# Kernel optimization log

Hardware: AMD Instinct MI355X
Metric: run time of the kernel (lower is better)

The kernel has to match this reference:

```python
import jax, jax.numpy as jnp
import numpy as np
import math

B, S, D, H, TD = 256, 200, 64, 512, 8


def setup_inputs():
    key = jax.random.key(0)
    ks = jax.random.split(key, 12)
    sd, sh, so = 1.0 / math.sqrt(D), 1.0 / math.sqrt(H), 1.0 / math.sqrt(H + TD)
    return dict(
        x=jax.random.normal(ks[0], (B, S, D), jnp.float32),
        a=jax.random.normal(ks[3], (B, TD), jnp.float32),
        t=jnp.cumsum(jax.random.uniform(ks[2], (B, S), jnp.float32), axis=1),
        mask=(jax.random.uniform(ks[1], (B, S, D)) < 0.8).astype(jnp.float32),
        w_dg_x=jax.random.normal(ks[4], (D,), jnp.float32) * sd,
        b_dg_x=jnp.zeros((D,), jnp.float32),
        W_dg_h=jax.random.normal(ks[5], (H, D), jnp.float32) * sd,
        b_dg_h=jnp.zeros((H,), jnp.float32),
        W=jax.random.normal(ks[6], (3 * H, D), jnp.float32) * sd,
        U=jax.random.normal(ks[7], (3 * H, H), jnp.float32) * sh,
        V=jax.random.normal(ks[8], (3 * H, D), jnp.float32) * sd,
        b=jnp.zeros((3 * H,), jnp.float32),
        attn_v=jnp.ones((H,), jnp.float32),
        W_out=jax.random.normal(ks[9], (H, H + TD), jnp.float32) * so,
        b_out=jnp.zeros((H,), jnp.float32),
    )


def reference(x, a, t, mask, w_dg_x, b_dg_x, W_dg_h, b_dg_h, W, U, V, b, attn_v, W_out, b_out):
    # ---- GRU-D preprocessing: per-feature time gaps delta ----
    x_tm = jnp.transpose(x, (1, 0, 2))    # (S,B,D) time-major
    m_tm = jnp.transpose(mask, (1, 0, 2))
    dt = jnp.diff(t, axis=1, prepend=t[:, :1])      # (B,S), dt[0]=0
    dt_tm = jnp.transpose(dt)[:, :, None]           # (S,B,1)
    # delta[i] = dt[i] + (1 - mask[i-1]) * delta[i-1]; ones at step 0 -> delta[0]=0
    m_prev = jnp.concatenate([jnp.ones((1,) + m_tm.shape[1:], m_tm.dtype), m_tm[:-1]], axis=0)

    def delta_step(d, inp):
        dt_i, mp_i = inp
        d = dt_i + (1.0 - mp_i) * d
        return d, d

    _, delta_tm = jax.lax.scan(delta_step, jnp.zeros((B, D), x.dtype), (dt_tm, m_prev))

    # empirical mean of observed values for imputation
    x_mean = (mask * x).sum((0, 1)) / jnp.maximum(mask.sum((0, 1)), 1.0)  # (D,)

    Wz, Wr, Wh = W[:H], W[H:2 * H], W[2 * H:]
    Uz, Ur, Uh = U[:H], U[H:2 * H], U[2 * H:]
    Vz, Vr, Vh = V[:H], V[H:2 * H], V[2 * H:]
    bz, br, bh = b[:H], b[H:2 * H], b[2 * H:]

    def cell(carry, inp):
        h, x_last = carry
        x_i, m_i, d_i = inp                                        # (B,D) each
        gamma_x = jnp.exp(-jax.nn.relu(w_dg_x * d_i + b_dg_x))     # (B,D) input decay
        gamma_h = jnp.exp(-jax.nn.relu(d_i @ W_dg_h.T + b_dg_h))   # (B,H) hidden decay
        x_hat = m_i * x_i + (1.0 - m_i) * (gamma_x * x_last + (1.0 - gamma_x) * x_mean)
        h_dec = gamma_h * h
        z = jax.nn.sigmoid(x_hat @ Wz.T + h_dec @ Uz.T + m_i @ Vz.T + bz)
        r = jax.nn.sigmoid(x_hat @ Wr.T + h_dec @ Ur.T + m_i @ Vr.T + br)
        h_til = jnp.tanh(x_hat @ Wh.T + (r * h_dec) @ Uh.T + m_i @ Vh.T + bh)
        h_new = (1.0 - z) * h_dec + z * h_til
        x_last_new = m_i * x_i + (1.0 - m_i) * x_last
        return (h_new, x_last_new), h_new

    init = (jnp.zeros((B, H), x.dtype), jnp.zeros((B, D), x.dtype))
    _, h_all = jax.lax.scan(cell, init, (x_tm, m_tm, delta_tm))    # (S,B,H)

    # ---- attention pooling over time (softmax along seq dim, as in torch dim=0) ----
    score = (h_all @ attn_v) / math.sqrt(H)        # (S,B)
    w_attn = jax.nn.softmax(score, axis=0)
    attn_h = (h_all * w_attn[..., None]).sum(0)    # (B,H)

    # ---- treatment head ----
    return jnp.concatenate([attn_h, a], axis=1) @ W_out.T + b_out  # (B,H)
```

## Files before the change

### kernel.cpp

```cpp
#include <hip/hip_runtime.h>
#include <hip/hip_bf16.h>
#include <stdint.h>


typedef unsigned short u16;
typedef unsigned int   u32;
typedef unsigned long long u64;
typedef short bfrag  __attribute__((ext_vector_type(8)));
typedef u16   u16x8  __attribute__((ext_vector_type(8)));
typedef float f32x4  __attribute__((ext_vector_type(4)));

#define NB 256
#define NS 200
#define ND 64
#define NH 512

#define MFMA(a,b,c) __builtin_amdgcn_mfma_f32_16x16x32_bf16((a),(b),(c),0,0,0)

union UQ { u16x8 h; bfrag s; u64 u[2]; uint4 q; };

__device__ __forceinline__ float b2f(u16 v){ union { float f; u32 u; } c; c.u = ((u32)v) << 16; return c.f; }
__device__ __forceinline__ u16 f2b(float f){ union { float f; u32 u; } c; c.f = f; u32 r = c.u + 0x7FFFu + ((c.u >> 16) & 1u); return (u16)(r >> 16); }
__device__ __forceinline__ float sigm(float x){ return 1.f / (1.f + __expf(-x)); }
__device__ __forceinline__ float tanh_f(float x){ return 1.f - 2.f / (1.f + __expf(2.f * x)); }

__device__ __forceinline__ u64 cload64(const void* p){
  return __hip_atomic_load((const u64*)p, __ATOMIC_RELAXED, __HIP_MEMORY_SCOPE_AGENT);
}
__device__ __forceinline__ void cstore64(void* p, u64 v){
  __hip_atomic_store((u64*)p, v, __ATOMIC_RELAXED, __HIP_MEMORY_SCOPE_AGENT);
}
__device__ __forceinline__ u32 cload32(const u32* p){
  return __hip_atomic_load(p, __ATOMIC_RELAXED, __HIP_MEMORY_SCOPE_AGENT);
}
__device__ __forceinline__ void cstore32(u32* p, u32 v){
  __hip_atomic_store(p, v, __ATOMIC_RELAXED, __HIP_MEMORY_SCOPE_AGENT);
}
__device__ __forceinline__ bool poll_ge(const u32* wp, u32 tgt){
  int fuel = 1 << 19;
  while (true) {
    u32 v = cload32(wp);
    if (__all(v >= tgt)) return true;
    __builtin_amdgcn_s_sleep(1);
    if (--fuel == 0) return false;
  }
}
__device__ __forceinline__ bfrag ldfrag(const float* src){
  f32x4 lo = *(const f32x4*)src;
  f32x4 hi = *(const f32x4*)(src + 4);
  UQ z;
  z.h[0]=f2b(lo[0]); z.h[1]=f2b(lo[1]); z.h[2]=f2b(lo[2]); z.h[3]=f2b(lo[3]);
  z.h[4]=f2b(hi[0]); z.h[5]=f2b(hi[1]); z.h[6]=f2b(hi[2]); z.h[7]=f2b(hi[3]);
  return z.s;
}
__device__ __forceinline__ void stage_bf16(u16* dst, const u16* src, int tid, bool zero){
  const int row = tid >> 4, sc = (tid & 15) * 32;
  u16* dp = &dst[((sc >> 3) * 16 + row) * 8];
  if (!zero) {
    const u16* hs = src + (size_t)row * 512 + sc;
    u64 a0 = cload64(hs),      a1 = cload64(hs + 4),  a2 = cload64(hs + 8),  a3 = cload64(hs + 12);
    u64 a4 = cload64(hs + 16), a5 = cload64(hs + 20), a6 = cload64(hs + 24), a7 = cload64(hs + 28);
    *(u64*)(dp)       = a0; *(u64*)(dp + 4)   = a1;
    *(u64*)(dp + 128) = a2; *(u64*)(dp + 132) = a3;
    *(u64*)(dp + 256) = a4; *(u64*)(dp + 260) = a5;
    *(u64*)(dp + 384) = a6; *(u64*)(dp + 388) = a7;
  } else {
    *(u64*)(dp)       = 0; *(u64*)(dp + 4)   = 0;
    *(u64*)(dp + 128) = 0; *(u64*)(dp + 132) = 0;
    *(u64*)(dp + 256) = 0; *(u64*)(dp + 260) = 0;
    *(u64*)(dp + 384) = 0; *(u64*)(dp + 388) = 0;
  }
}


__global__ void transpose_k(const float* __restrict__ Wout, float* __restrict__ WT){
  int i = blockIdx.x * 256 + threadIdx.x;
  if (i < 520 * 512) { int k = i >> 9, ho = i & 511; WT[i] = Wout[ho * 520 + k]; }
}

__global__ void mean1_k(const float* __restrict__ x, const float* __restrict__ mask,
                        float* __restrict__ PX, float* __restrict__ PM){
  int s = blockIdx.x, tid = threadIdx.x;
  __shared__ float lx[256], lm[256];
  float xa = 0.f, ma = 0.f;
  for (int i = tid; i < NB * ND; i += 256) {
    int b = i >> 6, d = i & 63;
    size_t ix = ((size_t)b * NS + s) * 64 + d;
    float m = mask[ix];
    xa += m * x[ix]; ma += m;
  }
  lx[tid] = xa; lm[tid] = ma;
  __syncthreads();
  if (tid < 64) {
    PX[(size_t)s * 64 + tid] = lx[tid] + lx[tid + 64] + lx[tid + 128] + lx[tid + 192];
    PM[(size_t)s * 64 + tid] = lm[tid] + lm[tid + 64] + lm[tid + 128] + lm[tid + 192];
  }
}

__global__ void mean2_k(const float* __restrict__ PX, const float* __restrict__ PM,
                        float* __restrict__ XMEAN){
  int d = threadIdx.x;
  float sx = 0.f, sm = 0.f;
  for (int s = 0; s < NS; ++s){ sx += PX[s * 64 + d]; sm += PM[s * 64 + d]; }
  XMEAN[d] = sx / fmaxf(sm, 1.f);
}

__global__ void prep_k(const float* __restrict__ x, const float* __restrict__ mask,
                       const float* __restrict__ tc, const float* __restrict__ wdgx,
                       const float* __restrict__ bdgx, const float* __restrict__ XMEAN,
                       u16* __restrict__ XHAT, u16* __restrict__ MASKB, u16* __restrict__ DELTA){
  int g = blockIdx.x * 256 + threadIdx.x;
  int b = g >> 6, d = g & 63;
  float xmean = XMEAN[d], wx = wdgx[d], bx = bdgx[d];
  float xl = 0.f, del = 0.f, tprev = 0.f, mprev = 1.f;
  for (int s = 0; s < NS; ++s){
    float tv = tc[b * NS + s];
    float dtv = (s == 0) ? 0.f : (tv - tprev);
    tprev = tv;
    del = dtv + (1.f - mprev) * del;
    size_t ix = ((size_t)b * NS + s) * 64 + d;
    float m = mask[ix], xv = x[ix];
    float gx = __expf(-fmaxf(0.f, wx * del + bx));
    float xh = m * xv + (1.f - m) * (gx * xl + (1.f - gx) * xmean);
    size_t ox = ((size_t)s * NB + b) * 64 + d;
    XHAT[ox] = f2b(xh); MASKB[ox] = f2b(m); DELTA[ox] = f2b(del);
    xl = m * xv + (1.f - m) * xl;
    mprev = m;
  }
}

__global__ void xpart_k(const float* __restrict__ Wm, const float* __restrict__ Vm,
                        const float* __restrict__ bv, const u16* __restrict__ XHAT,
                        const u16* __restrict__ MASKB, u16* __restrict__ XP){
  const int tid = threadIdx.x, lane = tid & 63, wid = tid >> 6;
  const int l16 = lane & 15, krow = lane >> 4, r4 = lane >> 2, cb = (lane & 3) * 8;
  const int chunk = blockIdx.x >> 1, p = blockIdx.x & 1;
  const int R0 = chunk * 128;
  const int wbase = p * 768 + wid * 192;
  __shared__ u16 panel[16 * 16 * 8];
  __shared__ float xb[4][16 * 35];
  float* xw = xb[wid];
  const f32x4 Z4 = {0.f, 0.f, 0.f, 0.f};

  bfrag BW[12][2], BV2[12][2];
  #pragma unroll
  for (int ct = 0; ct < 12; ++ct)
    #pragma unroll
    for (int kx = 0; kx < 2; ++kx) {
      BW[ct][kx]  = ldfrag(Wm + (size_t)(wbase + ct * 16 + l16) * 64 + kx * 32 + krow * 8);
      BV2[ct][kx] = ldfrag(Vm + (size_t)(wbase + ct * 16 + l16) * 64 + kx * 32 + krow * 8);
    }
  float bias6[6][8];
  #pragma unroll
  for (int grp = 0; grp < 6; ++grp)
    #pragma unroll
    for (int q = 0; q < 8; ++q) bias6[grp][q] = bv[wbase + grp * 32 + cb + q];

  for (int it = 0; it < 8; ++it) {
    const int R = R0 + it * 16;
    { const int kb = tid >> 4, row = tid & 15;
      const u16* sp = (kb < 8 ? XHAT : MASKB) + (size_t)(R + row) * 64 + (kb & 7) * 8;
      *(uint4*)&panel[(kb * 16 + row) * 8] = *(const uint4*)sp; }
    __syncthreads();
    u16* orow_ = XP + (size_t)(R + r4) * 1536 + wbase;
    #pragma unroll
    for (int grp = 0; grp < 6; ++grp) {
      f32x4 ac0 = Z4, ac1 = Z4;
      #pragma unroll
      for (int kx = 0; kx < 2; ++kx) {
        bfrag ax = *(const bfrag*)&panel[((kx * 4 + krow) * 16 + l16) * 8];
        ac0 = MFMA(ax, BW[grp*2][kx], ac0); ac1 = MFMA(ax, BW[grp*2+1][kx], ac1);
        bfrag am = *(const bfrag*)&panel[((8 + kx * 4 + krow) * 16 + l16) * 8];
        ac0 = MFMA(am, BV2[grp*2][kx], ac0); ac1 = MFMA(am, BV2[grp*2+1][kx], ac1);
      }
      #pragma unroll
      for (int j = 0; j < 4; ++j) { xw[(krow*4+j)*35 + l16] = ac0[j]; xw[(krow*4+j)*35 + 16 + l16] = ac1[j]; }
      UQ ov;
      #pragma unroll
      for (int q = 0; q < 8; ++q) ov.h[q] = f2b(xw[r4 * 35 + cb + q] + bias6[grp][q]);
      *(u64*)(orow_ + grp * 32 + cb) = ov.u[0];
      *(u64*)(orow_ + grp * 32 + cb + 4) = ov.u[1];
    }
    __syncthreads();
  }
}

__global__ __launch_bounds__(256, 1) void grud_rnn(
    const float* __restrict__ Um, const float* __restrict__ Wdg, const float* __restrict__ bdg,
    const u16* __restrict__ XP, const u16* __restrict__ DELTA,
    u16* __restrict__ HDECB, u16* __restrict__ RHB, u16* __restrict__ HALL,
    u32* __restrict__ flags)
{
  const int tid = threadIdx.x, lane = tid & 63, wid = tid >> 6, bid = blockIdx.x;
  const int lid = (bid & 7) * 8 + (bid >> 3);
  const int rb = lid >> 2, g = lid & 3, m0 = rb * 16;
  const int l16 = lane & 15, krow = lane >> 4, r4 = lane >> 2, cb = (lane & 3) * 8;
  const int pw = g * 4 + wid;
  const int cw = g * 128 + wid * 32;
  u32* FB = flags + rb * 32;

  __shared__ u16 hpan[64 * 16 * 8];
  __shared__ u16 rpan[64 * 16 * 8];
  __shared__ u16 dpan[8 * 16 * 8];
  __shared__ float xb[4][16 * 34];
  __shared__ int s_ab;
  float* xw = xb[wid];
  const f32x4 Z4 = {0.f, 0.f, 0.f, 0.f};
  if (tid == 0) s_ab = 0;
  __syncthreads();

  bfrag BZ[16][2], BR[16][2], BH[16][2], BG[2][2];
  #pragma unroll
  for (int kk = 0; kk < 16; ++kk) {
    const size_t ko = (size_t)(kk * 32 + krow * 8);
    #pragma unroll
    for (int t2 = 0; t2 < 2; ++t2) {
      BZ[kk][t2] = ldfrag(Um + (size_t)(       cw + t2 * 16 + l16) * 512 + ko);
      BR[kk][t2] = ldfrag(Um + (size_t)(512  + cw + t2 * 16 + l16) * 512 + ko);
      BH[kk][t2] = ldfrag(Um + (size_t)(1024 + cw + t2 * 16 + l16) * 512 + ko);
    }
  }
  #pragma unroll
  for (int kk = 0; kk < 2; ++kk)
    #pragma unroll
    for (int t2 = 0; t2 < 2; ++t2)
      BG[kk][t2] = ldfrag(Wdg + (size_t)(cw + t2 * 16 + l16) * 64 + kk * 32 + krow * 8);
  float gb8[8];
  #pragma unroll
  for (int q = 0; q < 8; ++q) gb8[q] = bdg[cw + cb + q];

  const int slot = ((cw + cb) >> 3) * 16 + r4;

  for (int t = 0; t < NS; ++t) {
    const int tn = (t + 1 < NS) ? t + 1 : NS - 1;
    const u16* xp = XP + ((size_t)t * NB + m0 + r4) * 1536 + cw + cb;
    u64 xz0 = *(const u64*)(xp),        xz1 = *(const u64*)(xp + 4);
    u64 xr0 = *(const u64*)(xp + 512),  xr1 = *(const u64*)(xp + 516);
    u64 xh0 = *(const u64*)(xp + 1024), xh1 = *(const u64*)(xp + 1028);
    if (tid < 128) {
      const int kb = tid >> 4, row = tid & 15;
      const u16* sp = DELTA + ((size_t)tn * NB + m0 + row) * 64 + kb * 8;
      *(uint4*)&dpan[(kb * 16 + row) * 8] = *(const uint4*)sp;
    }
    if (wid == 0 && t > 0) { if (!poll_ge(FB + (lane & 15), (u32)t)) s_ab = 1; }
    __syncthreads();
    if (s_ab) break;
    stage_bf16(hpan, HDECB + (size_t)m0 * 512, tid, t == 0);
    __syncthreads();
    f32x4 aR0 = Z4, aR1 = Z4;
    #pragma unroll
    for (int kk = 0; kk < 16; ++kk) {
      bfrag a = *(const bfrag*)&hpan[((kk * 4 + krow) * 16 + l16) * 8];
      aR0 = MFMA(a, BR[kk][0], aR0); aR1 = MFMA(a, BR[kk][1], aR1);
    }
    #pragma unroll
    for (int j = 0; j < 4; ++j) { xw[(krow*4+j)*34 + l16] = aR0[j]; xw[(krow*4+j)*34 + 16 + l16] = aR1[j]; }
    UQ hd_; hd_.h = *(const u16x8*)&hpan[slot * 8];
    UQ xr_; xr_.u[0] = xr0; xr_.u[1] = xr1;
    UQ rh_;
    #pragma unroll
    for (int q = 0; q < 8; ++q) {
      float rv = sigm(b2f(xr_.h[q]) + xw[r4 * 34 + cb + q]);
      rh_.h[q] = f2b(rv * b2f(hd_.h[q]));
    }
    u16* rdst = RHB + (size_t)(m0 + r4) * 512 + cw + cb;
    cstore64(rdst, rh_.u[0]); cstore64(rdst + 4, rh_.u[1]);
    asm volatile("s_waitcnt vmcnt(0)" ::: "memory");
    if (lane == 0) cstore32(FB + 16 + pw, (u32)(t + 1));
    f32x4 aZ0 = Z4, aZ1 = Z4;
    #pragma unroll
    for (int kk = 0; kk < 16; ++kk) {
      bfrag a = *(const bfrag*)&hpan[((kk * 4 + krow) * 16 + l16) * 8];
      aZ0 = MFMA(a, BZ[kk][0], aZ0); aZ1 = MFMA(a, BZ[kk][1], aZ1);
    }
    #pragma unroll
    for (int j = 0; j < 4; ++j) { xw[(krow*4+j)*34 + l16] = aZ0[j]; xw[(krow*4+j)*34 + 16 + l16] = aZ1[j]; }
    UQ xz_; xz_.u[0] = xz0; xz_.u[1] = xz1;
    float zf[8];
    #pragma unroll
    for (int q = 0; q < 8; ++q) zf[q] = sigm(b2f(xz_.h[q]) + xw[r4 * 34 + cb + q]);
    f32x4 g0 = Z4, g1 = Z4;
    #pragma unroll
    for (int kk = 0; kk < 2; ++kk) {
      bfrag a = *(const bfrag*)&dpan[((kk * 4 + krow) * 16 + l16) * 8];
      g0 = MFMA(a, BG[kk][0], g0); g1 = MFMA(a, BG[kk][1], g1);
    }
    #pragma unroll
    for (int j = 0; j < 4; ++j) { xw[(krow*4+j)*34 + l16] = g0[j]; xw[(krow*4+j)*34 + 16 + l16] = g1[j]; }
    float gm8[8];
    #pragma unroll
    for (int q = 0; q < 8; ++q)
      gm8[q] = __expf(-fmaxf(0.f, xw[r4 * 34 + cb + q] + gb8[q]));
    if (wid == 0) { if (!poll_ge(FB + 16 + (lane & 15), (u32)(t + 1))) s_ab = 1; }
    __syncthreads();
    if (s_ab) break;
    stage_bf16(rpan, RHB + (size_t)m0 * 512, tid, false);
    __syncthreads();
    f32x4 aH0 = Z4, aH1 = Z4;
    #pragma unroll
    for (int kk = 0; kk < 16; ++kk) {
      bfrag a = *(const bfrag*)&rpan[((kk * 4 + krow) * 16 + l16) * 8];
      aH0 = MFMA(a, BH[kk][0], aH0); aH1 = MFMA(a, BH[kk][1], aH1);
    }
    #pragma unroll
    for (int j = 0; j < 4; ++j) { xw[(krow*4+j)*34 + l16] = aH0[j]; xw[(krow*4+j)*34 + 16 + l16] = aH1[j]; }
    UQ xh_; xh_.u[0] = xh0; xh_.u[1] = xh1;
    UQ hw_, hdn_;
    #pragma unroll
    for (int q = 0; q < 8; ++q) {
      float til = tanh_f(b2f(xh_.h[q]) + xw[r4 * 34 + cb + q]);
      float hn = (1.f - zf[q]) * b2f(hd_.h[q]) + zf[q] * til;
      hw_.h[q] = f2b(hn);
      hdn_.h[q] = f2b(gm8[q] * hn);
    }
    if (t + 1 < NS) {
      u16* hdst = HDECB + (size_t)(m0 + r4) * 512 + cw + cb;
      cstore64(hdst, hdn_.u[0]); cstore64(hdst + 4, hdn_.u[1]);
    }
    asm volatile("s_waitcnt vmcnt(0)" ::: "memory");
    if (lane == 0) cstore32(FB + 0 + pw, (u32)(t + 1));
    u16* hp = HALL + ((size_t)t * NB + m0 + r4) * 512 + cw + cb;
    *(u64*)hp = hw_.u[0]; *(u64*)(hp + 4) = hw_.u[1];
    __syncthreads();
  }
}


__global__ void attn_k(const u16* __restrict__ HALL, const float* __restrict__ av,
                       float* __restrict__ ATTN){
  const int b = blockIdx.x, tid = threadIdx.x, lane = tid & 63, wid = tid >> 6;
  __shared__ float avs[512], wgt[256], red[8];
  for (int i = tid; i < 512; i += 256) avs[i] = av[i];
  __syncthreads();
  float val = -3.0e38f;
  if (tid < NS) {
    const u16* hp = HALL + ((size_t)tid * NB + b) * 512;
    float acc = 0.f;
    for (int h = 0; h < 512; h += 8) {
      UQ w; w.q = *(const uint4*)(hp + h);
      #pragma unroll
      for (int j = 0; j < 8; ++j) acc += b2f(w.h[j]) * avs[h + j];
    }
    val = acc * 0.04419417382415922f;
  }
  float m = val;
  #pragma unroll
  for (int off = 32; off; off >>= 1) m = fmaxf(m, __shfl_xor(m, off, 64));
  if (lane == 0) red[wid] = m;
  __syncthreads();
  m = fmaxf(fmaxf(red[0], red[1]), fmaxf(red[2], red[3]));
  float e = (tid < NS) ? __expf(val - m) : 0.f;
  float sum = e;
  #pragma unroll
  for (int off = 32; off; off >>= 1) sum += __shfl_xor(sum, off, 64);
  if (lane == 0) red[4 + wid] = sum;
  __syncthreads();
  const float ssum = red[4] + red[5] + red[6] + red[7];
  wgt[tid] = e / ssum;
  __syncthreads();
  float a0 = 0.f, a1 = 0.f;
  const int h0 = tid * 2;
  for (int s = 0; s < NS; ++s) {
    float w = wgt[s];
    u32 pr = *(const u32*)(HALL + ((size_t)s * NB + b) * 512 + h0);
    a0 += w * b2f((u16)(pr & 0xFFFFu));
    a1 += w * b2f((u16)(pr >> 16));
  }
  ATTN[(size_t)b * 512 + h0] = a0;
  ATTN[(size_t)b * 512 + h0 + 1] = a1;
}

__global__ void out_k(const float* __restrict__ ATTN, const float* __restrict__ Ain,
                      const float* __restrict__ WT, const float* __restrict__ bout,
                      float* __restrict__ OUT){
  const int g = blockIdx.x, tid = threadIdx.x;
  __shared__ float ah[4][520];
  for (int i = tid; i < 4 * 520; i += 256) {
    int bb = i / 520, k = i % 520;
    int b = g * 4 + bb;
    ah[bb][k] = (k < 512) ? ATTN[(size_t)b * 512 + k] : Ain[b * 8 + (k - 512)];
  }
  __syncthreads();
  #pragma unroll
  for (int part = 0; part < 2; ++part) {
    const int ho = part * 256 + tid;
    float a0 = bout[ho], a1 = a0, a2 = a0, a3 = a0;
    for (int k = 0; k < 520; ++k) {
      float w = WT[(size_t)k * 512 + ho];
      a0 += ah[0][k] * w; a1 += ah[1][k] * w; a2 += ah[2][k] * w; a3 += ah[3][k] * w;
    }
    OUT[(size_t)(g * 4 + 0) * 512 + ho] = a0;
    OUT[(size_t)(g * 4 + 1) * 512 + ho] = a1;
    OUT[(size_t)(g * 4 + 2) * 512 + ho] = a2;
    OUT[(size_t)(g * 4 + 3) * 512 + ho] = a3;
  }
}


extern "C" void kernel_launch(void* const* d_in, const int* in_sizes, int n_in,
                              void* d_out, int out_size, void* d_ws, size_t ws_size,
                              hipStream_t stream) {
  (void)in_sizes; (void)n_in; (void)out_size; (void)ws_size;
  const float* x    = (const float*)d_in[0];
  const float* a_in = (const float*)d_in[1];
  const float* tc   = (const float*)d_in[2];
  const float* mask = (const float*)d_in[3];
  const float* wdgx = (const float*)d_in[4];
  const float* bdgx = (const float*)d_in[5];
  const float* Wdgh = (const float*)d_in[6];
  const float* bdgh = (const float*)d_in[7];
  const float* Wm   = (const float*)d_in[8];
  const float* Um   = (const float*)d_in[9];
  const float* Vm   = (const float*)d_in[10];
  const float* bvv  = (const float*)d_in[11];
  const float* attv = (const float*)d_in[12];
  const float* Wout = (const float*)d_in[13];
  const float* bout = (const float*)d_in[14];

  char* ws = (char*)d_ws;
  size_t o = 0;
  auto al = [&](size_t sz) { size_t r = o; o += (sz + 255) & ~(size_t)255; return r; };
  u32*   flags = (u32*)  (ws + al(16 * 32 * 4));
  float* XMEAN = (float*)(ws + al(256));
  float* PX    = (float*)(ws + al((size_t)NS * 64 * 4));
  float* PM    = (float*)(ws + al((size_t)NS * 64 * 4));
  u16*   XHAT  = (u16*)  (ws + al((size_t)NS * NB * 64 * 2));
  u16*   MASKB = (u16*)  (ws + al((size_t)NS * NB * 64 * 2));
  u16*   DELTA = (u16*)  (ws + al((size_t)NS * NB * 64 * 2));
  u16*   HDECB = (u16*)  (ws + al((size_t)NB * NH * 2));
  u16*   RHB   = (u16*)  (ws + al((size_t)NB * NH * 2));
  u16*   XP    = (u16*)  (ws + al((size_t)NS * NB * 1536 * 2));
  u16*   HALL  = (u16*)  (ws + al((size_t)NS * NB * NH * 2));
  float* ATTN  = (float*)(ws + al((size_t)NB * NH * 4));
  float* WT    = (float*)(ws + al((size_t)520 * 512 * 4));

  hipMemsetAsync(flags, 0, 16 * 32 * 4, stream);

  transpose_k<<<(520 * 512 + 255) / 256, 256, 0, stream>>>(Wout, WT);
  mean1_k<<<NS, 256, 0, stream>>>(x, mask, PX, PM);
  mean2_k<<<1, 64, 0, stream>>>(PX, PM, XMEAN);
  prep_k<<<NB * ND / 256, 256, 0, stream>>>(x, mask, tc, wdgx, bdgx, XMEAN, XHAT, MASKB, DELTA);
  xpart_k<<<800, 256, 0, stream>>>(Wm, Vm, bvv, XHAT, MASKB, XP);
  grud_rnn<<<64, 256, 0, stream>>>(Um, Wdgh, bdgh, XP, DELTA, HDECB, RHB, HALL, flags);
  attn_k<<<NB, 256, 0, stream>>>(HALL, attv, ATTN);
  out_k<<<64, 256, 0, stream>>>(ATTN, a_in, WT, bout, (float*)d_out);
}
```

Measured before the change: 2.174 ms.

## Split z-gate GEMM onto dedicated blocks and read h/r panels directly from global

The persistent GRU-D recurrence kernel grows from 64 to 96 blocks. Per 16-row batch group, four blocks handle the r and candidate gates, and two new blocks compute the z gate in parallel, publishing it through a global buffer guarded by flags. Hidden and reset panels are stored pre-swizzled in MFMA fragment order and loaded straight into registers, which removes LDS staging and its barriers. Flag polling also drops the sleep instruction. The r/h blocks now wait on the z blocks before the candidate step, and the extra flag traffic could lengthen the critical path.

```diff
diff --git a/kernel.cpp b/kernel.cpp
--- a/kernel.cpp
+++ b/kernel.cpp
@@ -37,11 +37,10 @@
   __hip_atomic_store(p, v, __ATOMIC_RELAXED, __HIP_MEMORY_SCOPE_AGENT);
 }
 __device__ __forceinline__ bool poll_ge(const u32* wp, u32 tgt){
-  int fuel = 1 << 19;
+  int fuel = 1 << 18;
   while (true) {
     u32 v = cload32(wp);
     if (__all(v >= tgt)) return true;
-    __builtin_amdgcn_s_sleep(1);
     if (--fuel == 0) return false;
   }
 }
@@ -52,24 +51,6 @@
   z.h[0]=f2b(lo[0]); z.h[1]=f2b(lo[1]); z.h[2]=f2b(lo[2]); z.h[3]=f2b(lo[3]);
   z.h[4]=f2b(hi[0]); z.h[5]=f2b(hi[1]); z.h[6]=f2b(hi[2]); z.h[7]=f2b(hi[3]);
   return z.s;
-}
-__device__ __forceinline__ void stage_bf16(u16* dst, const u16* src, int tid, bool zero){
-  const int row = tid >> 4, sc = (tid & 15) * 32;
-  u16* dp = &dst[((sc >> 3) * 16 + row) * 8];
-  if (!zero) {
-    const u16* hs = src + (size_t)row * 512 + sc;
-    u64 a0 = cload64(hs),      a1 = cload64(hs + 4),  a2 = cload64(hs + 8),  a3 = cload64(hs + 12);
-    u64 a4 = cload64(hs + 16), a5 = cload64(hs + 20), a6 = cload64(hs + 24), a7 = cload64(hs + 28);
-    *(u64*)(dp)       = a0; *(u64*)(dp + 4)   = a1;
-    *(u64*)(dp + 128) = a2; *(u64*)(dp + 132) = a3;
-    *(u64*)(dp + 256) = a4; *(u64*)(dp + 260) = a5;
-    *(u64*)(dp + 384) = a6; *(u64*)(dp + 388) = a7;
-  } else {
-    *(u64*)(dp)       = 0; *(u64*)(dp + 4)   = 0;
-    *(u64*)(dp + 128) = 0; *(u64*)(dp + 132) = 0;
-    *(u64*)(dp + 256) = 0; *(u64*)(dp + 260) = 0;
-    *(u64*)(dp + 384) = 0; *(u64*)(dp + 388) = 0;
-  }
 }
 
 
@@ -188,140 +169,199 @@
 __global__ __launch_bounds__(256, 1) void grud_rnn(
     const float* __restrict__ Um, const float* __restrict__ Wdg, const float* __restrict__ bdg,
     const u16* __restrict__ XP, const u16* __restrict__ DELTA,
-    u16* __restrict__ HDECB, u16* __restrict__ RHB, u16* __restrict__ HALL,
-    u32* __restrict__ flags)
+    u16* __restrict__ HP, u16* __restrict__ RP, u16* __restrict__ ZZB,
+    u16* __restrict__ HALL, u32* __restrict__ flags)
 {
   const int tid = threadIdx.x, lane = tid & 63, wid = tid >> 6, bid = blockIdx.x;
-  const int lid = (bid & 7) * 8 + (bid >> 3);
-  const int rb = lid >> 2, g = lid & 3, m0 = rb * 16;
+  const int lid = (bid & 7) * 12 + (bid >> 3);
+  const int rb = lid / 6, role = lid % 6, m0 = rb * 16;
   const int l16 = lane & 15, krow = lane >> 4, r4 = lane >> 2, cb = (lane & 3) * 8;
-  const int pw = g * 4 + wid;
-  const int cw = g * 128 + wid * 32;
-  u32* FB = flags + rb * 32;
-
-  __shared__ u16 hpan[64 * 16 * 8];
-  __shared__ u16 rpan[64 * 16 * 8];
-  __shared__ u16 dpan[8 * 16 * 8];
-  __shared__ float xb[4][16 * 34];
-  __shared__ int s_ab;
+  u32* FB = flags + rb * 64;
+  u16* HPr = HP + rb * 8192;
+  u16* RPr = RP + rb * 8192;
+
+  __shared__ float xb[4][16 * 68];
   float* xw = xb[wid];
   const f32x4 Z4 = {0.f, 0.f, 0.f, 0.f};
-  if (tid == 0) s_ab = 0;
-  __syncthreads();
-
-  bfrag BZ[16][2], BR[16][2], BH[16][2], BG[2][2];
-  #pragma unroll
-  for (int kk = 0; kk < 16; ++kk) {
-    const size_t ko = (size_t)(kk * 32 + krow * 8);
-    #pragma unroll
-    for (int t2 = 0; t2 < 2; ++t2) {
-      BZ[kk][t2] = ldfrag(Um + (size_t)(       cw + t2 * 16 + l16) * 512 + ko);
-      BR[kk][t2] = ldfrag(Um + (size_t)(512  + cw + t2 * 16 + l16) * 512 + ko);
-      BH[kk][t2] = ldfrag(Um + (size_t)(1024 + cw + t2 * 16 + l16) * 512 + ko);
-    }
-  }
-  #pragma unroll
-  for (int kk = 0; kk < 2; ++kk)
-    #pragma unroll
-    for (int t2 = 0; t2 < 2; ++t2)
-      BG[kk][t2] = ldfrag(Wdg + (size_t)(cw + t2 * 16 + l16) * 64 + kk * 32 + krow * 8);
-  float gb8[8];
-  #pragma unroll
-  for (int q = 0; q < 8; ++q) gb8[q] = bdg[cw + cb + q];
-
-  const int slot = ((cw + cb) >> 3) * 16 + r4;
-
-  for (int t = 0; t < NS; ++t) {
-    const int tn = (t + 1 < NS) ? t + 1 : NS - 1;
-    const u16* xp = XP + ((size_t)t * NB + m0 + r4) * 1536 + cw + cb;
-    u64 xz0 = *(const u64*)(xp),        xz1 = *(const u64*)(xp + 4);
-    u64 xr0 = *(const u64*)(xp + 512),  xr1 = *(const u64*)(xp + 516);
-    u64 xh0 = *(const u64*)(xp + 1024), xh1 = *(const u64*)(xp + 1028);
-    if (tid < 128) {
-      const int kb = tid >> 4, row = tid & 15;
-      const u16* sp = DELTA + ((size_t)tn * NB + m0 + row) * 64 + kb * 8;
-      *(uint4*)&dpan[(kb * 16 + row) * 8] = *(const uint4*)sp;
-    }
-    if (wid == 0 && t > 0) { if (!poll_ge(FB + (lane & 15), (u32)t)) s_ab = 1; }
-    __syncthreads();
-    if (s_ab) break;
-    stage_bf16(hpan, HDECB + (size_t)m0 * 512, tid, t == 0);
-    __syncthreads();
-    f32x4 aR0 = Z4, aR1 = Z4;
+
+  if (role < 4) {
+    const int pw = role * 4 + wid;
+    const int cw = role * 128 + wid * 32;
+    const int slotp = ((cw + cb) >> 3) * 16 + r4;
+    bfrag BR[16][2], BH[16][2], BG[2][2];
     #pragma unroll
     for (int kk = 0; kk < 16; ++kk) {
-      bfrag a = *(const bfrag*)&hpan[((kk * 4 + krow) * 16 + l16) * 8];
-      aR0 = MFMA(a, BR[kk][0], aR0); aR1 = MFMA(a, BR[kk][1], aR1);
-    }
-    #pragma unroll
-    for (int j = 0; j < 4; ++j) { xw[(krow*4+j)*34 + l16] = aR0[j]; xw[(krow*4+j)*34 + 16 + l16] = aR1[j]; }
-    UQ hd_; hd_.h = *(const u16x8*)&hpan[slot * 8];
-    UQ xr_; xr_.u[0] = xr0; xr_.u[1] = xr1;
-    UQ rh_;
-    #pragma unroll
-    for (int q = 0; q < 8; ++q) {
-      float rv = sigm(b2f(xr_.h[q]) + xw[r4 * 34 + cb + q]);
-      rh_.h[q] = f2b(rv * b2f(hd_.h[q]));
-    }
-    u16* rdst = RHB + (size_t)(m0 + r4) * 512 + cw + cb;
-    cstore64(rdst, rh_.u[0]); cstore64(rdst + 4, rh_.u[1]);
-    asm volatile("s_waitcnt vmcnt(0)" ::: "memory");
-    if (lane == 0) cstore32(FB + 16 + pw, (u32)(t + 1));
-    f32x4 aZ0 = Z4, aZ1 = Z4;
-    #pragma unroll
-    for (int kk = 0; kk < 16; ++kk) {
-      bfrag a = *(const bfrag*)&hpan[((kk * 4 + krow) * 16 + l16) * 8];
-      aZ0 = MFMA(a, BZ[kk][0], aZ0); aZ1 = MFMA(a, BZ[kk][1], aZ1);
-    }
-    #pragma unroll
-    for (int j = 0; j < 4; ++j) { xw[(krow*4+j)*34 + l16] = aZ0[j]; xw[(krow*4+j)*34 + 16 + l16] = aZ1[j]; }
-    UQ xz_; xz_.u[0] = xz0; xz_.u[1] = xz1;
-    float zf[8];
-    #pragma unroll
-    for (int q = 0; q < 8; ++q) zf[q] = sigm(b2f(xz_.h[q]) + xw[r4 * 34 + cb + q]);
-    f32x4 g0 = Z4, g1 = Z4;
-    #pragma unroll
-    for (int kk = 0; kk < 2; ++kk) {
-      bfrag a = *(const bfrag*)&dpan[((kk * 4 + krow) * 16 + l16) * 8];
-      g0 = MFMA(a, BG[kk][0], g0); g1 = MFMA(a, BG[kk][1], g1);
-    }
-    #pragma unroll
-    for (int j = 0; j < 4; ++j) { xw[(krow*4+j)*34 + l16] = g0[j]; xw[(krow*4+j)*34 + 16 + l16] = g1[j]; }
-    float gm8[8];
-    #pragma unroll
-    for (int q = 0; q < 8; ++q)
-      gm8[q] = __expf(-fmaxf(0.f, xw[r4 * 34 + cb + q] + gb8[q]));
-    if (wid == 0) { if (!poll_ge(FB + 16 + (lane & 15), (u32)(t + 1))) s_ab = 1; }
-    __syncthreads();
-    if (s_ab) break;
-    stage_bf16(rpan, RHB + (size_t)m0 * 512, tid, false);
-    __syncthreads();
-    f32x4 aH0 = Z4, aH1 = Z4;
-    #pragma unroll
-    for (int kk = 0; kk < 16; ++kk) {
-      bfrag a = *(const bfrag*)&rpan[((kk * 4 + krow) * 16 + l16) * 8];
-      aH0 = MFMA(a, BH[kk][0], aH0); aH1 = MFMA(a, BH[kk][1], aH1);
-    }
-    #pragma unroll
-    for (int j = 0; j < 4; ++j) { xw[(krow*4+j)*34 + l16] = aH0[j]; xw[(krow*4+j)*34 + 16 + l16] = aH1[j]; }
-    UQ xh_; xh_.u[0] = xh0; xh_.u[1] = xh1;
-    UQ hw_, hdn_;
-    #pragma unroll
-    for (int q = 0; q < 8; ++q) {
-      float til = tanh_f(b2f(xh_.h[q]) + xw[r4 * 34 + cb + q]);
-      float hn = (1.f - zf[q]) * b2f(hd_.h[q]) + zf[q] * til;
-      hw_.h[q] = f2b(hn);
-      hdn_.h[q] = f2b(gm8[q] * hn);
-    }
-    if (t + 1 < NS) {
-      u16* hdst = HDECB + (size_t)(m0 + r4) * 512 + cw + cb;
-      cstore64(hdst, hdn_.u[0]); cstore64(hdst + 4, hdn_.u[1]);
-    }
-    asm volatile("s_waitcnt vmcnt(0)" ::: "memory");
-    if (lane == 0) cstore32(FB + 0 + pw, (u32)(t + 1));
-    u16* hp = HALL + ((size_t)t * NB + m0 + r4) * 512 + cw + cb;
-    *(u64*)hp = hw_.u[0]; *(u64*)(hp + 4) = hw_.u[1];
-    __syncthreads();
+      const size_t ko = (size_t)(kk * 32 + krow * 8);
+      #pragma unroll
+      for (int t2 = 0; t2 < 2; ++t2) {
+        BR[kk][t2] = ldfrag(Um + (size_t)(512  + cw + t2 * 16 + l16) * 512 + ko);
+        BH[kk][t2] = ldfrag(Um + (size_t)(1024 + cw + t2 * 16 + l16) * 512 + ko);
+      }
+    }
+    #pragma unroll
+    for (int kk = 0; kk < 2; ++kk)
+      #pragma unroll
+      for (int t2 = 0; t2 < 2; ++t2)
+        BG[kk][t2] = ldfrag(Wdg + (size_t)(cw + t2 * 16 + l16) * 64 + kk * 32 + krow * 8);
+    float gb8[8];
+    #pragma unroll
+    for (int q = 0; q < 8; ++q) gb8[q] = bdg[cw + cb + q];
+
+    UQ hd_; hd_.u[0] = 0; hd_.u[1] = 0;
+
+    for (int t = 0; t < NS; ++t) {
+      const int tn = (t + 1 < NS) ? t + 1 : NS - 1;
+      const u16* xp = XP + ((size_t)t * NB + m0 + r4) * 1536 + cw + cb;
+      u64 xr0 = *(const u64*)(xp + 512),  xr1 = *(const u64*)(xp + 516);
+      u64 xh0 = *(const u64*)(xp + 1024), xh1 = *(const u64*)(xp + 1028);
+      const u16* dpp = DELTA + ((size_t)tn * NB + m0 + l16) * 64 + krow * 8;
+      UQ DA[2];
+      DA[0].u[0] = *(const u64*)(dpp);      DA[0].u[1] = *(const u64*)(dpp + 4);
+      DA[1].u[0] = *(const u64*)(dpp + 32); DA[1].u[1] = *(const u64*)(dpp + 36);
+      if (t > 0) { if (!poll_ge(FB + (lane & 15), (u32)t)) return; }
+      UQ A[16];
+      if (t > 0) {
+        #pragma unroll
+        for (int kk = 0; kk < 16; ++kk) {
+          const u16* p = HPr + (size_t)(kk * 64 + krow * 16 + l16) * 8;
+          A[kk].u[0] = cload64(p); A[kk].u[1] = cload64(p + 4);
+        }
+      } else {
+        #pragma unroll
+        for (int kk = 0; kk < 16; ++kk) { A[kk].u[0] = 0; A[kk].u[1] = 0; }
+      }
+      f32x4 aR0 = Z4, aR1 = Z4;
+      #pragma unroll
+      for (int kk = 0; kk < 16; ++kk) {
+        aR0 = MFMA(A[kk].s, BR[kk][0], aR0); aR1 = MFMA(A[kk].s, BR[kk][1], aR1);
+      }
+      #pragma unroll
+      for (int j = 0; j < 4; ++j) { xw[(krow*4+j)*68 + l16] = aR0[j]; xw[(krow*4+j)*68 + 16 + l16] = aR1[j]; }
+      UQ xr_; xr_.u[0] = xr0; xr_.u[1] = xr1;
+      UQ rh_;
+      #pragma unroll
+      for (int q = 0; q < 8; ++q) {
+        float rv = sigm(b2f(xr_.h[q]) + xw[r4 * 68 + cb + q]);
+        rh_.h[q] = f2b(rv * b2f(hd_.h[q]));
+      }
+      { u16* rdst = RPr + (size_t)slotp * 8;
+        cstore64(rdst, rh_.u[0]); cstore64(rdst + 4, rh_.u[1]); }
+      asm volatile("s_waitcnt vmcnt(0)" ::: "memory");
+      if (lane == 0) cstore32(FB + 16 + pw, (u32)(t + 1));
+      f32x4 g0 = Z4, g1 = Z4;
+      #pragma unroll
+      for (int kk = 0; kk < 2; ++kk) {
+        g0 = MFMA(DA[kk].s, BG[kk][0], g0); g1 = MFMA(DA[kk].s, BG[kk][1], g1);
+      }
+      #pragma unroll
+      for (int j = 0; j < 4; ++j) { xw[(krow*4+j)*68 + l16] = g0[j]; xw[(krow*4+j)*68 + 16 + l16] = g1[j]; }
+      float gm8[8];
+      #pragma unroll
+      for (int q = 0; q < 8; ++q)
+        gm8[q] = __expf(-fmaxf(0.f, xw[r4 * 68 + cb + q] + gb8[q]));
+      { const u32* wp; u32 tg = (u32)(t + 1);
+        if (lane < 16)      wp = FB + 16 + lane;
+        else if (lane < 24) wp = FB + 32 + (lane - 16);
+        else                wp = FB + 16;
+        if (!poll_ge(wp, tg)) return; }
+      u64 zz0 = cload64(ZZB + (size_t)(m0 + r4) * 512 + cw + cb);
+      u64 zz1 = cload64(ZZB + (size_t)(m0 + r4) * 512 + cw + cb + 4);
+      #pragma unroll
+      for (int kk = 0; kk < 16; ++kk) {
+        const u16* p = RPr + (size_t)(kk * 64 + krow * 16 + l16) * 8;
+        A[kk].u[0] = cload64(p); A[kk].u[1] = cload64(p + 4);
+      }
+      f32x4 aH0 = Z4, aH1 = Z4;
+      #pragma unroll
+      for (int kk = 0; kk < 16; ++kk) {
+        aH0 = MFMA(A[kk].s, BH[kk][0], aH0); aH1 = MFMA(A[kk].s, BH[kk][1], aH1);
+      }
+      #pragma unroll
+      for (int j = 0; j < 4; ++j) { xw[(krow*4+j)*68 + l16] = aH0[j]; xw[(krow*4+j)*68 + 16 + l16] = aH1[j]; }
+      UQ xh_; xh_.u[0] = xh0; xh_.u[1] = xh1;
+      UQ zz_; zz_.u[0] = zz0; zz_.u[1] = zz1;
+      UQ hw_, hdn_;
+      #pragma unroll
+      for (int q = 0; q < 8; ++q) {
+        float til = tanh_f(b2f(xh_.h[q]) + xw[r4 * 68 + cb + q]);
+        float z = b2f(zz_.h[q]);
+        float hn = (1.f - z) * b2f(hd_.h[q]) + z * til;
+        hw_.h[q] = f2b(hn);
+        hdn_.h[q] = f2b(gm8[q] * hn);
+      }
+      if (t + 1 < NS) {
+        u16* hdst = HPr + (size_t)slotp * 8;
+        cstore64(hdst, hdn_.u[0]); cstore64(hdst + 4, hdn_.u[1]);
+      }
+      asm volatile("s_waitcnt vmcnt(0)" ::: "memory");
+      if (lane == 0) cstore32(FB + 0 + pw, (u32)(t + 1));
+      hd_ = hdn_;
+      u16* hp = HALL + ((size_t)t * NB + m0 + r4) * 512 + cw + cb;
+      *(u64*)hp = hw_.u[0]; *(u64*)(hp + 4) = hw_.u[1];
+    }
+  } else {
+    const int zi = role - 4;
+    const int pz = zi * 4 + wid;
+    const int zc = zi * 256 + wid * 64;
+    const int cb2 = (lane & 3) * 16;
+    bfrag BZ[16][4];
+    #pragma unroll
+    for (int kk = 0; kk < 16; ++kk)
+      #pragma unroll
+      for (int ct = 0; ct < 4; ++ct)
+        BZ[kk][ct] = ldfrag(Um + (size_t)(zc + ct * 16 + l16) * 512 + kk * 32 + krow * 8);
+
+    for (int t = 0; t < NS; ++t) {
+      const u16* xp = XP + ((size_t)t * NB + m0 + r4) * 1536 + zc + cb2;
+      u64 xz[4];
+      #pragma unroll
+      for (int c = 0; c < 4; ++c) xz[c] = *(const u64*)(xp + c * 4);
+      if (t > 0) { if (!poll_ge(FB + (lane & 15), (u32)t)) return; }
+      UQ A[16];
+      if (t > 0) {
+        #pragma unroll
+        for (int kk = 0; kk < 16; ++kk) {
+          const u16* p = HP + (size_t)rb * 8192 + (size_t)(kk * 64 + krow * 16 + l16) * 8;
+          A[kk].u[0] = cload64(p); A[kk].u[1] = cload64(p + 4);
+        }
+      } else {
+        #pragma unroll
+        for (int kk = 0; kk < 16; ++kk) { A[kk].u[0] = 0; A[kk].u[1] = 0; }
+      }
+      f32x4 acc[4] = {Z4, Z4, Z4, Z4};
+      #pragma unroll
+      for (int kk = 0; kk < 16; ++kk) {
+        #pragma unroll
+        for (int ct = 0; ct < 4; ++ct) acc[ct] = MFMA(A[kk].s, BZ[kk][ct], acc[ct]);
+      }
+      #pragma unroll
+      for (int ct = 0; ct < 4; ++ct)
+        #pragma unroll
+        for (int j = 0; j < 4; ++j)
+          xw[(krow * 4 + j) * 68 + ct * 16 + l16] = acc[ct][j];
+      UQ z0, z1;
+      #pragma unroll
+      for (int q = 0; q < 8; ++q) {
+        UQ xzq; xzq.u[0] = xz[q >> 2];
+      }
+      float s16[16];
+      #pragma unroll
+      for (int q = 0; q < 16; ++q) s16[q] = xw[r4 * 68 + cb2 + q];
+      UQ zo[2];
+      #pragma unroll
+      for (int c = 0; c < 2; ++c) {
+        UQ xa; xa.u[0] = xz[c * 2]; xa.u[1] = xz[c * 2 + 1];
+        UQ ov;
+        #pragma unroll
+        for (int q = 0; q < 8; ++q) ov.h[q] = f2b(sigm(b2f(xa.h[q]) + s16[c * 8 + q]));
+        zo[c] = ov;
+      }
+      u16* zdst = ZZB + (size_t)(m0 + r4) * 512 + zc + cb2;
+      cstore64(zdst, zo[0].u[0]); cstore64(zdst + 4, zo[0].u[1]);
+      cstore64(zdst + 8, zo[1].u[0]); cstore64(zdst + 12, zo[1].u[1]);
+      asm volatile("s_waitcnt vmcnt(0)" ::: "memory");
+      if (lane == 0) cstore32(FB + 32 + pz, (u32)(t + 1));
+    }
   }
 }
 
@@ -420,28 +460,29 @@
   char* ws = (char*)d_ws;
   size_t o = 0;
   auto al = [&](size_t sz) { size_t r = o; o += (sz + 255) & ~(size_t)255; return r; };
-  u32*   flags = (u32*)  (ws + al(16 * 32 * 4));
+  u32*   flags = (u32*)  (ws + al(16 * 64 * 4));
   float* XMEAN = (float*)(ws + al(256));
   float* PX    = (float*)(ws + al((size_t)NS * 64 * 4));
   float* PM    = (float*)(ws + al((size_t)NS * 64 * 4));
   u16*   XHAT  = (u16*)  (ws + al((size_t)NS * NB * 64 * 2));
   u16*   MASKB = (u16*)  (ws + al((size_t)NS * NB * 64 * 2));
   u16*   DELTA = (u16*)  (ws + al((size_t)NS * NB * 64 * 2));
-  u16*   HDECB = (u16*)  (ws + al((size_t)NB * NH * 2));
-  u16*   RHB   = (u16*)  (ws + al((size_t)NB * NH * 2));
+  u16*   HP    = (u16*)  (ws + al((size_t)16 * 8192 * 2));
+  u16*   RP    = (u16*)  (ws + al((size_t)16 * 8192 * 2));
+  u16*   ZZB   = (u16*)  (ws + al((size_t)NB * NH * 2));
   u16*   XP    = (u16*)  (ws + al((size_t)NS * NB * 1536 * 2));
   u16*   HALL  = (u16*)  (ws + al((size_t)NS * NB * NH * 2));
   float* ATTN  = (float*)(ws + al((size_t)NB * NH * 4));
   float* WT    = (float*)(ws + al((size_t)520 * 512 * 4));
 
-  hipMemsetAsync(flags, 0, 16 * 32 * 4, stream);
+  hipMemsetAsync(flags, 0, 16 * 64 * 4, stream);
 
   transpose_k<<<(520 * 512 + 255) / 256, 256, 0, stream>>>(Wout, WT);
   mean1_k<<<NS, 256, 0, stream>>>(x, mask, PX, PM);
   mean2_k<<<1, 64, 0, stream>>>(PX, PM, XMEAN);
   prep_k<<<NB * ND / 256, 256, 0, stream>>>(x, mask, tc, wdgx, bdgx, XMEAN, XHAT, MASKB, DELTA);
   xpart_k<<<800, 256, 0, stream>>>(Wm, Vm, bvv, XHAT, MASKB, XP);
-  grud_rnn<<<64, 256, 0, stream>>>(Um, Wdgh, bdgh, XP, DELTA, HDECB, RHB, HALL, flags);
+  grud_rnn<<<96, 256, 0, stream>>>(Um, Wdgh, bdgh, XP, DELTA, HP, RP, ZZB, HALL, flags);
   attn_k<<<NB, 256, 0, stream>>>(HALL, attv, ATTN);
   out_k<<<64, 256, 0, stream>>>(ATTN, a_in, WT, bout, (float*)d_out);
 }
```

Measured after the change: 2.650 ms. 1.22x slower.

## Store HALL batch-major, coalesce attention reads and stage xpart outputs in LDS

Applied to the files above, without the earlier changes.

The RNN now writes its hidden-state history batch-major (B,S,H) instead of time-major, so each attention block reads one contiguous slab. The attention score pass now has each wave compute full dot products with lane-parallel 16-byte loads and shuffle reductions, replacing the one-thread-per-timestep strided loop. xpart_k first stages its bf16 outputs in a shared-memory tile and then writes full rows with 16-byte coalesced stores, which costs extra LDS and an added barrier. The RNN's scattered per-step HALL stores may coalesce less well than before.

```diff
diff --git a/kernel.cpp b/kernel.cpp
--- a/kernel.cpp
+++ b/kernel.cpp
@@ -129,15 +129,18 @@
   }
 }
 
-__global__ void xpart_k(const float* __restrict__ Wm, const float* __restrict__ Vm,
-                        const float* __restrict__ bv, const u16* __restrict__ XHAT,
-                        const u16* __restrict__ MASKB, u16* __restrict__ XP){
+__global__ __launch_bounds__(256, 1) void xpart_k(
+    const float* __restrict__ Wm, const float* __restrict__ Vm,
+    const float* __restrict__ bv, const u16* __restrict__ XHAT,
+    const u16* __restrict__ MASKB, u16* __restrict__ XP){
   const int tid = threadIdx.x, lane = tid & 63, wid = tid >> 6;
   const int l16 = lane & 15, krow = lane >> 4, r4 = lane >> 2, cb = (lane & 3) * 8;
   const int chunk = blockIdx.x >> 1, p = blockIdx.x & 1;
   const int R0 = chunk * 128;
-  const int wbase = p * 768 + wid * 192;
+  const int wbasel = wid * 192;
+  const int wbaseg = p * 768 + wbasel;
   __shared__ u16 panel[16 * 16 * 8];
+  __shared__ u16 outs[16][768];
   __shared__ float xb[4][16 * 35];
   float* xw = xb[wid];
   const f32x4 Z4 = {0.f, 0.f, 0.f, 0.f};
@@ -147,14 +150,14 @@
   for (int ct = 0; ct < 12; ++ct)
     #pragma unroll
     for (int kx = 0; kx < 2; ++kx) {
-      BW[ct][kx]  = ldfrag(Wm + (size_t)(wbase + ct * 16 + l16) * 64 + kx * 32 + krow * 8);
-      BV2[ct][kx] = ldfrag(Vm + (size_t)(wbase + ct * 16 + l16) * 64 + kx * 32 + krow * 8);
+      BW[ct][kx]  = ldfrag(Wm + (size_t)(wbaseg + ct * 16 + l16) * 64 + kx * 32 + krow * 8);
+      BV2[ct][kx] = ldfrag(Vm + (size_t)(wbaseg + ct * 16 + l16) * 64 + kx * 32 + krow * 8);
     }
   float bias6[6][8];
   #pragma unroll
   for (int grp = 0; grp < 6; ++grp)
     #pragma unroll
-    for (int q = 0; q < 8; ++q) bias6[grp][q] = bv[wbase + grp * 32 + cb + q];
+    for (int q = 0; q < 8; ++q) bias6[grp][q] = bv[wbaseg + grp * 32 + cb + q];
 
   for (int it = 0; it < 8; ++it) {
     const int R = R0 + it * 16;
@@ -162,7 +165,6 @@
       const u16* sp = (kb < 8 ? XHAT : MASKB) + (size_t)(R + row) * 64 + (kb & 7) * 8;
       *(uint4*)&panel[(kb * 16 + row) * 8] = *(const uint4*)sp; }
     __syncthreads();
-    u16* orow_ = XP + (size_t)(R + r4) * 1536 + wbase;
     #pragma unroll
     for (int grp = 0; grp < 6; ++grp) {
       f32x4 ac0 = Z4, ac1 = Z4;
@@ -178,8 +180,14 @@
       UQ ov;
       #pragma unroll
       for (int q = 0; q < 8; ++q) ov.h[q] = f2b(xw[r4 * 35 + cb + q] + bias6[grp][q]);
-      *(u64*)(orow_ + grp * 32 + cb) = ov.u[0];
-      *(u64*)(orow_ + grp * 32 + cb + 4) = ov.u[1];
+      *(u64*)&outs[r4][wbasel + grp * 32 + cb] = ov.u[0];
+      *(u64*)&outs[r4][wbasel + grp * 32 + cb + 4] = ov.u[1];
+    }
+    __syncthreads();
+    for (int c = tid; c < 16 * 96; c += 256) {
+      const int row = c / 96, ch = c % 96;
+      *(uint4*)(XP + (size_t)(R + row) * 1536 + p * 768 + ch * 8) =
+          *(const uint4*)&outs[row][ch * 8];
     }
     __syncthreads();
   }
@@ -319,30 +327,33 @@
     }
     asm volatile("s_waitcnt vmcnt(0)" ::: "memory");
     if (lane == 0) cstore32(FB + 0 + pw, (u32)(t + 1));
-    u16* hp = HALL + ((size_t)t * NB + m0 + r4) * 512 + cw + cb;
+    u16* hp = HALL + ((size_t)(m0 + r4) * NS + t) * 512 + cw + cb;
     *(u64*)hp = hw_.u[0]; *(u64*)(hp + 4) = hw_.u[1];
     __syncthreads();
   }
 }
 
 
-__global__ void attn_k(const u16* __restrict__ HALL, const float* __restrict__ av,
-                       float* __restrict__ ATTN){
+__global__ __launch_bounds__(256) void attn_k(const u16* __restrict__ HALL,
+                                              const float* __restrict__ av,
+                                              float* __restrict__ ATTN){
   const int b = blockIdx.x, tid = threadIdx.x, lane = tid & 63, wid = tid >> 6;
-  __shared__ float avs[512], wgt[256], red[8];
+  __shared__ float avs[512], sc[256], wgt[256], red[8];
   for (int i = tid; i < 512; i += 256) avs[i] = av[i];
   __syncthreads();
-  float val = -3.0e38f;
-  if (tid < NS) {
-    const u16* hp = HALL + ((size_t)tid * NB + b) * 512;
-    float acc = 0.f;
-    for (int h = 0; h < 512; h += 8) {
-      UQ w; w.q = *(const uint4*)(hp + h);
-      #pragma unroll
-      for (int j = 0; j < 8; ++j) acc += b2f(w.h[j]) * avs[h + j];
-    }
-    val = acc * 0.04419417382415922f;
-  }
+  const u16* base = HALL + (size_t)b * NS * 512;
+  for (int i = 0; i < 50; ++i) {
+    const int s = wid * 50 + i;
+    UQ w8; w8.q = *(const uint4*)(base + (size_t)s * 512 + lane * 8);
+    float p = 0.f;
+    #pragma unroll
+    for (int j = 0; j < 8; ++j) p += b2f(w8.h[j]) * avs[lane * 8 + j];
+    #pragma unroll
+    for (int off = 32; off; off >>= 1) p += __shfl_xor(p, off, 64);
+    if (lane == 0) sc[s] = p * 0.04419417382415922f;
+  }
+  __syncthreads();
+  float val = (tid < NS) ? sc[tid] : -3.0e38f;
   float m = val;
   #pragma unroll
   for (int off = 32; off; off >>= 1) m = fmaxf(m, __shfl_xor(m, off, 64));
@@ -361,8 +372,8 @@
   float a0 = 0.f, a1 = 0.f;
   const int h0 = tid * 2;
   for (int s = 0; s < NS; ++s) {
-    float w = wgt[s];
-    u32 pr = *(const u32*)(HALL + ((size_t)s * NB + b) * 512 + h0);
+    const float w = wgt[s];
+    u32 pr = *(const u32*)(base + (size_t)s * 512 + h0);
     a0 += w * b2f((u16)(pr & 0xFFFFu));
     a1 += w * b2f((u16)(pr >> 16));
   }
```

Result: faster. 1.872 ms (-13.9%).
